# Performance work log

Hardware: AMD Instinct MI355X
Metric: run time of the kernel (lower is better)

## Reference

```python
import jax, jax.numpy as jnp
import numpy as np

# Model dims
B, S, H = 1, 1024, 2048
NH, NKV, DH = 32, 8, 64
G = NH // NKV            # GQA group size
E, K, I = 8, 2, 2048     # experts, top_k, intermediate
ALPHA, LIMIT = 1.702, 7.0
EPS = 1e-5
SCALE = DH ** -0.5


def rmsnorm(x, g):
    return x * jax.lax.rsqrt(jnp.mean(x * x, axis=-1, keepdims=True) + EPS) * g


def setup_inputs() -> dict:
    key = jax.random.key(0)
    ks = jax.random.split(key, 24)
    w = lambda k, shp: jax.random.normal(k, shp, dtype=jnp.float32) * 0.02
    causal = jnp.where(jnp.tril(jnp.ones((S, S), dtype=bool)), 0.0, -1e9).astype(jnp.float32)
    return {
        "hidden_states": jax.random.normal(ks[0], (B, S, H), dtype=jnp.float32),
        "attention_bias": causal[None, None, :, :],           # [1,1,S,S]
        "ln1_g": jnp.ones((H,), jnp.float32),
        "ln2_g": jnp.ones((H,), jnp.float32),
        "Wq": w(ks[1], (NH * DH, H)),  "bq": w(ks[2], (NH * DH,)),
        "Wk": w(ks[3], (NKV * DH, H)), "bk": w(ks[4], (NKV * DH,)),
        "Wv": w(ks[5], (NKV * DH, H)), "bv": w(ks[6], (NKV * DH,)),
        "Wo": w(ks[7], (H, NH * DH)),  "bo": w(ks[8], (H,)),
        "sinks": w(ks[9], (NH,)),
        "router_w": w(ks[10], (E, H)), "router_b": w(ks[11], (E,)),
        "We_gate": w(ks[12], (E, I, H)), "be_gate": w(ks[13], (E, I)),
        "We_up":   w(ks[14], (E, I, H)), "be_up":   w(ks[15], (E, I)),
        "We_down": w(ks[16], (E, H, I)), "be_down": w(ks[17], (E, H)),
    }


def reference(hidden_states, attention_bias, ln1_g, ln2_g,
              Wq, bq, Wk, bk, Wv, bv, Wo, bo, sinks,
              router_w, router_b,
              We_gate, be_gate, We_up, be_up, We_down, be_down):
    x = hidden_states
    # ---- pre-norm sink attention ----
    xn = rmsnorm(x, ln1_g)
    q = (xn @ Wq.T + bq).reshape(B, S, NH, DH).transpose(0, 2, 1, 3)    # [B,NH,S,DH]
    k = (xn @ Wk.T + bk).reshape(B, S, NKV, DH).transpose(0, 2, 1, 3)   # [B,NKV,S,DH]
    v = (xn @ Wv.T + bv).reshape(B, S, NKV, DH).transpose(0, 2, 1, 3)
    # GQA: replicate each kv head G times consecutively (repeat_kv)
    k = jnp.repeat(k, G, axis=1)
    v = jnp.repeat(v, G, axis=1)
    scores = jnp.einsum('bhqd,bhkd->bhqk', q, k) * SCALE + attention_bias  # [B,NH,S,S]
    sink_col = jnp.broadcast_to(sinks.reshape(1, NH, 1, 1), (B, NH, S, 1))
    combined = jnp.concatenate([scores, sink_col], axis=-1)               # [B,NH,S,S+1]
    probs = jax.nn.softmax(combined, axis=-1)[..., :-1]                   # drop sink
    attn = jnp.einsum('bhqk,bhkd->bhqd', probs, v)
    attn = attn.transpose(0, 2, 1, 3).reshape(B, S, NH * DH)
    h = x + (attn @ Wo.T + bo)
    # ---- pre-norm MoE FFN ----
    hn = rmsnorm(h, ln2_g)
    router_logits = hn @ router_w.T + router_b                            # [B,S,E]
    rw, sel = jax.lax.top_k(router_logits, K)
    rw = jax.nn.softmax(rw, axis=-1)                                      # [B,S,K]
    # dense per-expert MLP over all tokens (matches the exported loop)
    gate = jnp.einsum('bsh,eih->bsei', hn, We_gate) + be_gate             # [B,S,E,I]
    up = jnp.einsum('bsh,eih->bsei', hn, We_up) + be_up
    gate_c = jnp.minimum(gate, LIMIT)
    up_c = jnp.clip(up, -LIMIT, LIMIT)
    glu = gate_c * jax.nn.sigmoid(ALPHA * gate_c)
    gated = (up_c + 1.0) * glu
    down = jnp.einsum('bsei,ehi->bseh', gated, We_down) + be_down         # [B,S,E,H]
    # per-token expert weight: sum_k rw * (sel == e)
    wts = jnp.sum(rw[..., None] * (sel[..., None] == jnp.arange(E)), axis=2)  # [B,S,E]
    moe = jnp.einsum('bseh,bse->bsh', down, wts)
    return h + moe
```

## Files before the change

### kernel.cpp

```cpp
#include <hip/hip_runtime.h>
#include <hip/hip_bf16.h>

#define HD 2048
#define SEQ 1024
#define NHEAD 32
#define NKVH 8
#define DHEAD 64
#define NEXP 8
#define INTER 2048
#define SCALE 0.125f
#define ALPHA 1.702f
#define LIMIT 7.0f

typedef __attribute__((ext_vector_type(8))) short short8;
typedef __attribute__((ext_vector_type(4))) short short4v;
typedef __attribute__((ext_vector_type(4))) float f32x4;

__device__ __forceinline__ unsigned short f2bf(float f) {
  union { float f; unsigned u; } v; v.f = f;
  unsigned r = v.u + 0x7fffu + ((v.u >> 16) & 1u);
  return (unsigned short)(r >> 16);
}
__device__ __forceinline__ float bf2f(unsigned short h) {
  union { unsigned u; float f; } v; v.u = ((unsigned)h) << 16; return v.f;
}
__device__ __forceinline__ void split2(float f, unsigned short& hi, unsigned short& lo) {
  hi = f2bf(f);
  lo = f2bf(f - bf2f(hi));
}

__device__ __forceinline__ f32x4 mfma32(short8 a, short8 b, f32x4 c) {
  return __builtin_amdgcn_mfma_f32_16x16x32_bf16(a, b, c, 0, 0, 0);
}

__global__ __launch_bounds__(256) void rmsnorm_split_kernel(
    const float* __restrict__ x, const float* __restrict__ gamma,
    unsigned short* __restrict__ oh, unsigned short* __restrict__ ol) {
  int row = blockIdx.x, tid = threadIdx.x;
  const float* xr = x + (size_t)row * HD;
  float v[8];
#pragma unroll
  for (int i = 0; i < 8; ++i) v[i] = xr[tid * 8 + i];
  float ss = 0.f;
#pragma unroll
  for (int i = 0; i < 8; ++i) ss += v[i] * v[i];
#pragma unroll
  for (int off = 32; off; off >>= 1) ss += __shfl_xor(ss, off, 64);
  __shared__ float wss[4];
  if ((tid & 63) == 0) wss[tid >> 6] = ss;
  __syncthreads();
  float rs = rsqrtf((wss[0] + wss[1] + wss[2] + wss[3]) * (1.0f / HD) + 1e-5f);
  short8 vh, vl;
#pragma unroll
  for (int i = 0; i < 8; ++i) {
    float val = v[i] * rs * gamma[tid * 8 + i];
    unsigned short h, lo;
    split2(val, h, lo);
    vh[i] = (short)h;
    vl[i] = (short)lo;
  }
  *(short8*)(oh + (size_t)row * HD + tid * 8) = vh;
  *(short8*)(ol + (size_t)row * HD + tid * 8) = vl;
}

__global__ __launch_bounds__(256) void rmsnorm_plain_kernel(
    const float* __restrict__ x, const float* __restrict__ gamma,
    unsigned short* __restrict__ out) {
  int row = blockIdx.x, tid = threadIdx.x;
  const float* xr = x + (size_t)row * HD;
  float v[8];
#pragma unroll
  for (int i = 0; i < 8; ++i) v[i] = xr[tid * 8 + i];
  float ss = 0.f;
#pragma unroll
  for (int i = 0; i < 8; ++i) ss += v[i] * v[i];
#pragma unroll
  for (int off = 32; off; off >>= 1) ss += __shfl_xor(ss, off, 64);
  __shared__ float wss[4];
  if ((tid & 63) == 0) wss[tid >> 6] = ss;
  __syncthreads();
  float rs = rsqrtf((wss[0] + wss[1] + wss[2] + wss[3]) * (1.0f / HD) + 1e-5f);
  short8 o;
#pragma unroll
  for (int i = 0; i < 8; ++i) o[i] = (short)f2bf(v[i] * rs * gamma[tid * 8 + i]);
  *(short8*)(out + (size_t)row * HD + tid * 8) = o;
}

template <int MT, int NS, bool SPLIT, int EPI>
__global__ __launch_bounds__(256) void gemm_ws(
    const unsigned short* __restrict__ Ah, const unsigned short* __restrict__ Al,
    int ldA,
    const float* __restrict__ W0, const float* __restrict__ W1,
    const float* __restrict__ W2,
    const float* __restrict__ b0, const float* __restrict__ b1,
    const float* __restrict__ b2,
    const float* __restrict__ resid,
    const int* __restrict__ counts, const int* __restrict__ arows,
    const int* __restrict__ orows,
    unsigned short* __restrict__ oh0, unsigned short* __restrict__ ol0,
    unsigned short* __restrict__ oh1, unsigned short* __restrict__ ol1,
    unsigned short* __restrict__ oh2, unsigned short* __restrict__ ol2,
    float* __restrict__ f0, float* __restrict__ f1,
    int M, int Kd) {
  constexpr int MG = MT * 64;
  constexpr int NR = NS * 16;
  constexpr int TPR = 256 / NR;
  constexpr int CPT = 128 / TPR;
  constexpr int NF4 = CPT / 4;
  constexpr int NPL = SPLIT ? 2 : 1;
  __shared__ __align__(16) unsigned short lw[2][NPL][NR][136];
  int tid = threadIdx.x;
  int l = tid & 63, w = tid >> 6;
  int g = l >> 4, q = l & 15;
  int n0 = blockIdx.x * NR;

  const float* Wb;
  const float* bias;
  int nloc = n0, e = 0, mat = 0;
  if constexpr (EPI == 0) {
    if (n0 < NHEAD * DHEAD) {
      Wb = W0; bias = b0;
    } else if (n0 < NHEAD * DHEAD + NKVH * DHEAD) {
      Wb = W1; bias = b1; nloc = n0 - NHEAD * DHEAD;
    } else {
      Wb = W2; bias = b2; nloc = n0 - (NHEAD * DHEAD + NKVH * DHEAD);
    }
  } else if constexpr (EPI == 1) {
    Wb = W0; bias = b0;
  } else if constexpr (EPI == 2) {
    e = blockIdx.z >> 1;
    mat = blockIdx.z & 1;
    Wb = (mat ? W1 : W0) + (size_t)e * INTER * HD;
    bias = (mat ? b1 : b0) + (size_t)e * INTER;
  } else {
    e = blockIdx.z;
    Wb = W0 + (size_t)e * HD * INTER;
    bias = b0 + (size_t)e * HD;
  }
  int cnt = (EPI >= 2) ? counts[e] : M;
  const float* wrow = Wb + (size_t)(nloc + tid / TPR) * Kd + (tid % TPR) * CPT;
  int wcc = (tid % TPR) * CPT;
  int wrr = tid / TPR;

  float4 wpre[NF4];
  auto stage = [&](int buf) {
#pragma unroll
    for (int j = 0; j < NF4; j += 2) {
      float v[8] = {wpre[j].x,     wpre[j].y,     wpre[j].z,     wpre[j].w,
                    wpre[j + 1].x, wpre[j + 1].y, wpre[j + 1].z, wpre[j + 1].w};
      short8 hh, ll;
#pragma unroll
      for (int jj = 0; jj < 8; ++jj) {
        if constexpr (SPLIT) {
          unsigned short h, lo;
          split2(v[jj], h, lo);
          hh[jj] = (short)h;
          ll[jj] = (short)lo;
        } else {
          hh[jj] = (short)f2bf(v[jj]);
        }
      }
      *(short8*)&lw[buf][0][wrr][wcc + j * 4] = hh;
      if constexpr (SPLIT) *(short8*)&lw[buf][NPL - 1][wrr][wcc + j * 4] = ll;
    }
  };

  for (int mg = blockIdx.y; mg * MG < cnt; mg += gridDim.y) {
    int mb = mg * MG + w * (MT * 16);
    const unsigned short* ap[MT];
    const unsigned short* apl[MT];
#pragma unroll
    for (int mt = 0; mt < MT; ++mt) {
      int mm = min(mb + mt * 16 + q, cnt - 1);
      int ar = (EPI >= 2) ? arows[e * SEQ + mm] : mm;
      ap[mt] = Ah + (size_t)ar * ldA + 8 * g;
      if constexpr (SPLIT) apl[mt] = Al + (size_t)ar * ldA + 8 * g;
    }
    f32x4 acc[MT][NS];
#pragma unroll
    for (int mt = 0; mt < MT; ++mt)
#pragma unroll
      for (int ns = 0; ns < NS; ++ns) acc[mt][ns] = (f32x4){0.f, 0.f, 0.f, 0.f};

#pragma unroll
    for (int j = 0; j < NF4; ++j) wpre[j] = *(const float4*)(wrow + 4 * j);
    short8 ab[2][MT], abl[2][MT];
#pragma unroll
    for (int mt = 0; mt < MT; ++mt) {
      ab[0][mt] = *(const short8*)(ap[mt]);
      ab[1][mt] = *(const short8*)(ap[mt] + 32);
      if constexpr (SPLIT) {
        abl[0][mt] = *(const short8*)(apl[mt]);
        abl[1][mt] = *(const short8*)(apl[mt] + 32);
      }
    }
    stage(0);
    __syncthreads();

    int cb = 0;
    for (int kc = 0; kc < Kd; kc += 128, cb ^= 1) {
      bool more = (kc + 128 < Kd);
      if (more) {
#pragma unroll
        for (int j = 0; j < NF4; ++j)
          wpre[j] = *(const float4*)(wrow + kc + 128 + 4 * j);
      }
#pragma unroll
      for (int kh = 0; kh < 4; ++kh) {
        short8 acur[MT], acl[MT];
#pragma unroll
        for (int mt = 0; mt < MT; ++mt) {
          acur[mt] = ab[kh & 1][mt];
          if constexpr (SPLIT) acl[mt] = abl[kh & 1][mt];
        }
        int kn = kc + kh * 32 + 64;
        if (kn < Kd) {
#pragma unroll
          for (int mt = 0; mt < MT; ++mt) {
            ab[kh & 1][mt] = *(const short8*)(ap[mt] + kn);
            if constexpr (SPLIT) abl[kh & 1][mt] = *(const short8*)(apl[mt] + kn);
          }
        }
        short8 wh[NS], wl[NS];
#pragma unroll
        for (int ns = 0; ns < NS; ++ns) {
          wh[ns] = *(const short8*)&lw[cb][0][ns * 16 + q][kh * 32 + 8 * g];
          if constexpr (SPLIT)
            wl[ns] = *(const short8*)&lw[cb][NPL - 1][ns * 16 + q][kh * 32 + 8 * g];
        }
#pragma unroll
        for (int mt = 0; mt < MT; ++mt)
#pragma unroll
          for (int ns = 0; ns < NS; ++ns) {
            acc[mt][ns] = mfma32(acur[mt], wh[ns], acc[mt][ns]);
            if constexpr (SPLIT) {
              acc[mt][ns] = mfma32(acur[mt], wl[ns], acc[mt][ns]);
              acc[mt][ns] = mfma32(acl[mt], wh[ns], acc[mt][ns]);
            }
          }
      }
      if (more) stage(cb ^ 1);
      __syncthreads();
    }
#pragma unroll
    for (int ns = 0; ns < NS; ++ns) {
      int ncol = nloc + ns * 16 + q;
      float bs = bias[ncol];
#pragma unroll
      for (int mt = 0; mt < MT; ++mt) {
#pragma unroll
        for (int r = 0; r < 4; ++r) {
          int mr = mb + mt * 16 + 4 * g + r;
          float val = acc[mt][ns][r] + bs;
          if constexpr (EPI == 0) {
            unsigned short h, lo;
            split2(val, h, lo);
            if (n0 < NHEAD * DHEAD) {
              oh0[(size_t)mr * (NHEAD * DHEAD) + ncol] = h;
              ol0[(size_t)mr * (NHEAD * DHEAD) + ncol] = lo;
            } else if (n0 < NHEAD * DHEAD + NKVH * DHEAD) {
              oh1[(size_t)mr * (NKVH * DHEAD) + ncol] = h;
              ol1[(size_t)mr * (NKVH * DHEAD) + ncol] = lo;
            } else {
              oh2[(size_t)ncol * SEQ + mr] = h;
              ol2[(size_t)ncol * SEQ + mr] = lo;
            }
          } else if constexpr (EPI == 1) {
            f0[(size_t)mr * HD + ncol] = val + resid[(size_t)mr * HD + ncol];
          } else if constexpr (EPI == 2) {
            if (mr < cnt) {
              int slot = orows[e * SEQ + mr];
              (mat ? f1 : f0)[(size_t)slot * INTER + ncol] = val;
            }
          } else {
            if (mr < cnt) {
              int slot = orows[e * SEQ + mr];
              f0[(size_t)slot * HD + ncol] = val;
            }
          }
        }
      }
    }
  }
}

__global__ __launch_bounds__(256) void attn_kernel(
    const unsigned short* __restrict__ Qh, const unsigned short* __restrict__ Ql,
    const unsigned short* __restrict__ Kh, const unsigned short* __restrict__ Kl,
    const unsigned short* __restrict__ Vh, const unsigned short* __restrict__ Vl,
    const float* __restrict__ sinks, unsigned short* __restrict__ outh,
    unsigned short* __restrict__ outl) {
  __shared__ __align__(16) unsigned short pbuf[4][2][16][40];
  int l = threadIdx.x & 63, widx = threadIdx.x >> 6;
  int wid = blockIdx.x * 4 + widx;
  int head = wid >> 6, qt = wid & 63;
  int q0 = qt * 16;
  int g = l >> 4, q = l & 15;
  int kvh = head >> 2;
  size_t qoff = (size_t)(q0 + q) * (NHEAD * DHEAD) + head * DHEAD + 8 * g;
  short8 qh0 = *(const short8*)(Qh + qoff);
  short8 qh1 = *(const short8*)(Qh + qoff + 32);
  short8 ql0 = *(const short8*)(Ql + qoff);
  short8 ql1 = *(const short8*)(Ql + qoff + 32);
  float m = sinks[head];
  float lsum = 1.0f;
  f32x4 o[4] = {{0, 0, 0, 0}, {0, 0, 0, 0}, {0, 0, 0, 0}, {0, 0, 0, 0}};
  int qglob = q0 + q;
  for (int kt = 0; kt <= qt; kt += 2) {
    bool hasB = (kt + 1) <= qt;
    size_t koff = (size_t)(kt * 16 + q) * (NKVH * DHEAD) + kvh * DHEAD + 8 * g;
    f32x4 stA = {0, 0, 0, 0};
    {
      short8 kh0 = *(const short8*)(Kh + koff);
      short8 kh1 = *(const short8*)(Kh + koff + 32);
      short8 kl0 = *(const short8*)(Kl + koff);
      short8 kl1 = *(const short8*)(Kl + koff + 32);
      stA = mfma32(kh0, qh0, stA);
      stA = mfma32(kh0, ql0, stA);
      stA = mfma32(kl0, qh0, stA);
      stA = mfma32(kh1, qh1, stA);
      stA = mfma32(kh1, ql1, stA);
      stA = mfma32(kl1, qh1, stA);
    }
    f32x4 stB = {0, 0, 0, 0};
    if (hasB) {
      size_t koff2 = koff + (size_t)16 * (NKVH * DHEAD);
      short8 kh0 = *(const short8*)(Kh + koff2);
      short8 kh1 = *(const short8*)(Kh + koff2 + 32);
      short8 kl0 = *(const short8*)(Kl + koff2);
      short8 kl1 = *(const short8*)(Kl + koff2 + 32);
// ... 173 lines not shown
}

extern "C" void kernel_launch(void* const* d_in, const int* in_sizes, int n_in,
                              void* d_out, int out_size, void* d_ws,
                              size_t ws_size, hipStream_t stream) {
  const float* x = (const float*)d_in[0];
  const float* ln1 = (const float*)d_in[2];
  const float* ln2 = (const float*)d_in[3];
  const float* Wq = (const float*)d_in[4];
  const float* bq = (const float*)d_in[5];
  const float* Wk = (const float*)d_in[6];
  const float* bk = (const float*)d_in[7];
  const float* Wv = (const float*)d_in[8];
  const float* bv = (const float*)d_in[9];
  const float* Wo = (const float*)d_in[10];
  const float* bo = (const float*)d_in[11];
  const float* sinks = (const float*)d_in[12];
  const float* rw = (const float*)d_in[13];
  const float* rb = (const float*)d_in[14];
  const float* Wg = (const float*)d_in[15];
  const float* bg = (const float*)d_in[16];
  const float* Wu = (const float*)d_in[17];
  const float* bu = (const float*)d_in[18];
  const float* Wd = (const float*)d_in[19];
  const float* bd = (const float*)d_in[20];
  float* out = (float*)d_out;

  char* ws = (char*)d_ws;
  size_t off = 0;
  auto alloc = [&](size_t bytes) {
    void* p = ws + off;
    off += (bytes + 255) & ~(size_t)255;
    return p;
  };
  unsigned short* xnh = (unsigned short*)alloc((size_t)SEQ * HD * 2);
  unsigned short* xnl = (unsigned short*)alloc((size_t)SEQ * HD * 2);
  unsigned short* qbh = (unsigned short*)alloc((size_t)SEQ * NHEAD * DHEAD * 2);
  unsigned short* qbl = (unsigned short*)alloc((size_t)SEQ * NHEAD * DHEAD * 2);
  unsigned short* kbh = (unsigned short*)alloc((size_t)SEQ * NKVH * DHEAD * 2);
  unsigned short* kbl = (unsigned short*)alloc((size_t)SEQ * NKVH * DHEAD * 2);
  unsigned short* vth = (unsigned short*)alloc((size_t)NKVH * DHEAD * SEQ * 2);
  unsigned short* vtl = (unsigned short*)alloc((size_t)NKVH * DHEAD * SEQ * 2);
  unsigned short* ath = (unsigned short*)alloc((size_t)SEQ * NHEAD * DHEAD * 2);
  unsigned short* atl = (unsigned short*)alloc((size_t)SEQ * NHEAD * DHEAD * 2);
  float* hbuf = (float*)alloc((size_t)SEQ * HD * 4);
  unsigned short* hn = (unsigned short*)alloc((size_t)SEQ * HD * 2);
  float* wsel = (float*)alloc((size_t)SEQ * 2 * 4);
  int* counts = (int*)alloc(NEXP * 4);
  int* lists = (int*)alloc((size_t)NEXP * SEQ * 4);
  int* slotof = (int*)alloc((size_t)NEXP * SEQ * 4);
  float* rawg = (float*)alloc((size_t)2 * SEQ * INTER * 4);
  float* rawu = (float*)alloc((size_t)2 * SEQ * INTER * 4);
  unsigned short* gated = (unsigned short*)alloc((size_t)2 * SEQ * INTER * 2);
  float* scr = rawg;
  (void)ws_size;
  (void)off;

  rmsnorm_split_kernel<<<SEQ, 256, 0, stream>>>(x, ln1, xnh, xnl);
  gemm_ws<4, 2, true, 0><<<dim3(96, 4, 1), 256, 0, stream>>>(
      xnh, xnl, HD, Wq, Wk, Wv, bq, bk, bv, nullptr, nullptr, nullptr, nullptr,
      qbh, qbl, kbh, kbl, vth, vtl, nullptr, nullptr, SEQ, HD);
  attn_kernel<<<NHEAD * 64 / 4, 256, 0, stream>>>(qbh, qbl, kbh, kbl, vth, vtl,
                                                  sinks, ath, atl);
  gemm_ws<4, 2, true, 1><<<dim3(64, 4, 1), 256, 0, stream>>>(
      ath, atl, NHEAD * DHEAD, Wo, nullptr, nullptr, bo, nullptr, nullptr, x,
      nullptr, nullptr, nullptr, nullptr, nullptr, nullptr, nullptr, nullptr,
      nullptr, hbuf, nullptr, SEQ, NHEAD * DHEAD);
  rmsnorm_plain_kernel<<<SEQ, 256, 0, stream>>>(hbuf, ln2, hn);
  hipMemsetAsync(counts, 0, NEXP * sizeof(int), stream);
  router_kernel<<<SEQ, 64, 0, stream>>>(hbuf, ln2, rw, rb, wsel, counts, lists,
                                        slotof);
  gemm_ws<5, 2, false, 2><<<dim3(64, 1, 16), 256, 0, stream>>>(
      hn, nullptr, HD, Wg, Wu, nullptr, bg, bu, nullptr, nullptr, counts, lists,
      slotof, nullptr, nullptr, nullptr, nullptr, nullptr, nullptr, rawg, rawu,
      SEQ, HD);
  act_kernel<<<2 * SEQ, 256, 0, stream>>>(rawg, rawu, gated);
  gemm_ws<5, 2, false, 3><<<dim3(64, 1, 8), 256, 0, stream>>>(
      gated, nullptr, INTER, Wd, nullptr, nullptr, bd, nullptr, nullptr,
      nullptr, counts, slotof, slotof, nullptr, nullptr, nullptr, nullptr,
      nullptr, nullptr, scr, nullptr, SEQ, INTER);
  reduce_kernel<<<SEQ, 256, 0, stream>>>(hbuf, scr, wsel, out);
}
```

Baseline: 663.6 us.

## Pre-convert weights to bf16 and split-K the MoE down projection with atomics

Adds conversion kernels that turn the fp32 weights into bf16 (hi/lo pairs for the attention projections) each call, so the GEMMs load half-width weights without converting inside the kernel. The GEMM inner loop now prefetches two weight chunks into registers with double buffering. The MoE GEMM tiles are widened. The down projection is split across two K halves that accumulate with atomicAdd into a zeroed buffer. The conversion passes add a full extra read and write of all weights on every call, which may cost more than the in-kernel conversion they replace.

```diff
diff --git a/kernel.cpp b/kernel.cpp
--- a/kernel.cpp
+++ b/kernel.cpp
@@ -33,6 +33,35 @@
   return __builtin_amdgcn_mfma_f32_16x16x32_bf16(a, b, c, 0, 0, 0);
 }
 
+__global__ __launch_bounds__(256) void conv_plain(const float* __restrict__ s,
+                                                  unsigned short* __restrict__ d) {
+  size_t i = ((size_t)blockIdx.x * 256 + threadIdx.x) * 8;
+  float4 a = *(const float4*)(s + i), b = *(const float4*)(s + i + 4);
+  float v[8] = {a.x, a.y, a.z, a.w, b.x, b.y, b.z, b.w};
+  short8 o;
+#pragma unroll
+  for (int j = 0; j < 8; ++j) o[j] = (short)f2bf(v[j]);
+  *(short8*)(d + i) = o;
+}
+
+__global__ __launch_bounds__(256) void conv_split(const float* __restrict__ s,
+                                                  unsigned short* __restrict__ dh,
+                                                  unsigned short* __restrict__ dl) {
+  size_t i = ((size_t)blockIdx.x * 256 + threadIdx.x) * 8;
+  float4 a = *(const float4*)(s + i), b = *(const float4*)(s + i + 4);
+  float v[8] = {a.x, a.y, a.z, a.w, b.x, b.y, b.z, b.w};
+  short8 oh, ol;
+#pragma unroll
+  for (int j = 0; j < 8; ++j) {
+    unsigned short h, lo;
+    split2(v[j], h, lo);
+    oh[j] = (short)h;
+    ol[j] = (short)lo;
+  }
+  *(short8*)(dh + i) = oh;
+  *(short8*)(dl + i) = ol;
+}
+
 __global__ __launch_bounds__(256) void rmsnorm_split_kernel(
     const float* __restrict__ x, const float* __restrict__ gamma,
     unsigned short* __restrict__ oh, unsigned short* __restrict__ ol) {
@@ -90,8 +119,9 @@
 __global__ __launch_bounds__(256) void gemm_ws(
     const unsigned short* __restrict__ Ah, const unsigned short* __restrict__ Al,
     int ldA,
-    const float* __restrict__ W0, const float* __restrict__ W1,
-    const float* __restrict__ W2,
+    const unsigned short* __restrict__ W0h, const unsigned short* __restrict__ W0l,
+    const unsigned short* __restrict__ W1h, const unsigned short* __restrict__ W1l,
+    const unsigned short* __restrict__ W2h, const unsigned short* __restrict__ W2l,
     const float* __restrict__ b0, const float* __restrict__ b1,
     const float* __restrict__ b2,
     const float* __restrict__ resid,
@@ -101,12 +131,12 @@
     unsigned short* __restrict__ oh1, unsigned short* __restrict__ ol1,
     unsigned short* __restrict__ oh2, unsigned short* __restrict__ ol2,
     float* __restrict__ f0, float* __restrict__ f1,
-    int M, int Kd) {
+    int M, int Kd, int Kr) {
   constexpr int MG = MT * 64;
   constexpr int NR = NS * 16;
   constexpr int TPR = 256 / NR;
   constexpr int CPT = 128 / TPR;
-  constexpr int NF4 = CPT / 4;
+  constexpr int NW8 = CPT / 8;
   constexpr int NPL = SPLIT ? 2 : 1;
   __shared__ __align__(16) unsigned short lw[2][NPL][NR][136];
   int tid = threadIdx.x;
@@ -114,58 +144,56 @@
   int g = l >> 4, q = l & 15;
   int n0 = blockIdx.x * NR;
 
-  const float* Wb;
+  const unsigned short* Wbh;
+  const unsigned short* Wbl = nullptr;
   const float* bias;
   int nloc = n0, e = 0, mat = 0;
   if constexpr (EPI == 0) {
     if (n0 < NHEAD * DHEAD) {
-      Wb = W0; bias = b0;
+      Wbh = W0h; Wbl = W0l; bias = b0;
     } else if (n0 < NHEAD * DHEAD + NKVH * DHEAD) {
-      Wb = W1; bias = b1; nloc = n0 - NHEAD * DHEAD;
+      Wbh = W1h; Wbl = W1l; bias = b1; nloc = n0 - NHEAD * DHEAD;
     } else {
-      Wb = W2; bias = b2; nloc = n0 - (NHEAD * DHEAD + NKVH * DHEAD);
+      Wbh = W2h; Wbl = W2l; bias = b2; nloc = n0 - (NHEAD * DHEAD + NKVH * DHEAD);
     }
   } else if constexpr (EPI == 1) {
-    Wb = W0; bias = b0;
+    Wbh = W0h; Wbl = W0l; bias = b0;
   } else if constexpr (EPI == 2) {
     e = blockIdx.z >> 1;
     mat = blockIdx.z & 1;
-    Wb = (mat ? W1 : W0) + (size_t)e * INTER * HD;
+    Wbh = (mat ? W1h : W0h) + (size_t)e * INTER * HD;
     bias = (mat ? b1 : b0) + (size_t)e * INTER;
   } else {
     e = blockIdx.z;
-    Wb = W0 + (size_t)e * HD * INTER;
+    Wbh = W0h + (size_t)e * HD * INTER;
     bias = b0 + (size_t)e * HD;
   }
   int cnt = (EPI >= 2) ? counts[e] : M;
-  const float* wrow = Wb + (size_t)(nloc + tid / TPR) * Kd + (tid % TPR) * CPT;
-  int wcc = (tid % TPR) * CPT;
-  int wrr = tid / TPR;
-
-  float4 wpre[NF4];
-  auto stage = [&](int buf) {
-#pragma unroll
-    for (int j = 0; j < NF4; j += 2) {
-      float v[8] = {wpre[j].x,     wpre[j].y,     wpre[j].z,     wpre[j].w,
-                    wpre[j + 1].x, wpre[j + 1].y, wpre[j + 1].z, wpre[j + 1].w};
-      short8 hh, ll;
-#pragma unroll
-      for (int jj = 0; jj < 8; ++jj) {
-        if constexpr (SPLIT) {
-          unsigned short h, lo;
-          split2(v[jj], h, lo);
-          hh[jj] = (short)h;
-          ll[jj] = (short)lo;
-        } else {
-          hh[jj] = (short)f2bf(v[jj]);
-        }
-      }
-      *(short8*)&lw[buf][0][wrr][wcc + j * 4] = hh;
-      if constexpr (SPLIT) *(short8*)&lw[buf][NPL - 1][wrr][wcc + j * 4] = ll;
+  int kstart = (EPI == 3) ? blockIdx.y * Kr : 0;
+  int mstart = (EPI <= 1) ? blockIdx.y : 0;
+  int mstep = (EPI <= 1) ? gridDim.y : 1;
+  int wrr = tid / TPR, wcc = (tid % TPR) * CPT;
+  const unsigned short* wrowh = Wbh + (size_t)(nloc + wrr) * Kd + kstart + wcc;
+  const unsigned short* wrowl =
+      SPLIT ? (Wbl + (size_t)(nloc + wrr) * Kd + kstart + wcc) : nullptr;
+
+  short8 wr[2][NW8], wrl[2][NW8];
+  auto loadW = [&](short8(&dh)[NW8], short8(&dl)[NW8], int kc) {
+#pragma unroll
+    for (int j = 0; j < NW8; ++j) {
+      dh[j] = *(const short8*)(wrowh + kc + j * 8);
+      if constexpr (SPLIT) dl[j] = *(const short8*)(wrowl + kc + j * 8);
     }
   };
-
-  for (int mg = blockIdx.y; mg * MG < cnt; mg += gridDim.y) {
+  auto stage = [&](int buf, short8(&sh)[NW8], short8(&sl)[NW8]) {
+#pragma unroll
+    for (int j = 0; j < NW8; ++j) {
+      *(short8*)&lw[buf][0][wrr][wcc + j * 8] = sh[j];
+      if constexpr (SPLIT) *(short8*)&lw[buf][NPL - 1][wrr][wcc + j * 8] = sl[j];
+    }
+  };
+
+  for (int mg = mstart; mg * MG < cnt; mg += mstep) {
     int mb = mg * MG + w * (MT * 16);
     const unsigned short* ap[MT];
     const unsigned short* apl[MT];
@@ -173,8 +201,8 @@
     for (int mt = 0; mt < MT; ++mt) {
       int mm = min(mb + mt * 16 + q, cnt - 1);
       int ar = (EPI >= 2) ? arows[e * SEQ + mm] : mm;
-      ap[mt] = Ah + (size_t)ar * ldA + 8 * g;
-      if constexpr (SPLIT) apl[mt] = Al + (size_t)ar * ldA + 8 * g;
+      ap[mt] = Ah + (size_t)ar * ldA + kstart + 8 * g;
+      if constexpr (SPLIT) apl[mt] = Al + (size_t)ar * ldA + kstart + 8 * g;
     }
     f32x4 acc[MT][NS];
 #pragma unroll
@@ -182,8 +210,8 @@
 #pragma unroll
       for (int ns = 0; ns < NS; ++ns) acc[mt][ns] = (f32x4){0.f, 0.f, 0.f, 0.f};
 
-#pragma unroll
-    for (int j = 0; j < NF4; ++j) wpre[j] = *(const float4*)(wrow + 4 * j);
+    loadW(wr[0], wrl[0], 0);
+    loadW(wr[1], wrl[1], 128);
     short8 ab[2][MT], abl[2][MT];
 #pragma unroll
     for (int mt = 0; mt < MT; ++mt) {
@@ -194,58 +222,60 @@
         abl[1][mt] = *(const short8*)(apl[mt] + 32);
       }
     }
-    stage(0);
+    stage(0, wr[0], wrl[0]);
     __syncthreads();
 
-    int cb = 0;
-    for (int kc = 0; kc < Kd; kc += 128, cb ^= 1) {
-      bool more = (kc + 128 < Kd);
-      if (more) {
-#pragma unroll
-        for (int j = 0; j < NF4; ++j)
-          wpre[j] = *(const float4*)(wrow + kc + 128 + 4 * j);
-      }
-#pragma unroll
-      for (int kh = 0; kh < 4; ++kh) {
-        short8 acur[MT], acl[MT];
-#pragma unroll
-        for (int mt = 0; mt < MT; ++mt) {
-          acur[mt] = ab[kh & 1][mt];
-          if constexpr (SPLIT) acl[mt] = abl[kh & 1][mt];
-        }
-        int kn = kc + kh * 32 + 64;
-        if (kn < Kd) {
+    for (int kc = 0; kc < Kr; kc += 256) {
+#pragma unroll
+      for (int u = 0; u < 2; ++u) {
+        int kcc = kc + u * 128;
+        if (kcc + 256 < Kr) loadW(wr[u], wrl[u], kcc + 256);
+#pragma unroll
+        for (int kh = 0; kh < 4; ++kh) {
+          short8 acur[MT], acl[MT];
 #pragma unroll
           for (int mt = 0; mt < MT; ++mt) {
-            ab[kh & 1][mt] = *(const short8*)(ap[mt] + kn);
-            if constexpr (SPLIT) abl[kh & 1][mt] = *(const short8*)(apl[mt] + kn);
+            acur[mt] = ab[kh & 1][mt];
+            if constexpr (SPLIT) acl[mt] = abl[kh & 1][mt];
           }
-        }
-        short8 wh[NS], wl[NS];
-#pragma unroll
-        for (int ns = 0; ns < NS; ++ns) {
-          wh[ns] = *(const short8*)&lw[cb][0][ns * 16 + q][kh * 32 + 8 * g];
-          if constexpr (SPLIT)
-            wl[ns] = *(const short8*)&lw[cb][NPL - 1][ns * 16 + q][kh * 32 + 8 * g];
-        }
-#pragma unroll
-        for (int mt = 0; mt < MT; ++mt)
-#pragma unroll
-          for (int ns = 0; ns < NS; ++ns) {
-            acc[mt][ns] = mfma32(acur[mt], wh[ns], acc[mt][ns]);
-            if constexpr (SPLIT) {
-              acc[mt][ns] = mfma32(acur[mt], wl[ns], acc[mt][ns]);
-              acc[mt][ns] = mfma32(acl[mt], wh[ns], acc[mt][ns]);
+          int kn = kcc + kh * 32 + 64;
+          if (kn < Kr) {
+#pragma unroll
+            for (int mt = 0; mt < MT; ++mt) {
+              ab[kh & 1][mt] = *(const short8*)(ap[mt] + kn);
+              if constexpr (SPLIT)
+                abl[kh & 1][mt] = *(const short8*)(apl[mt] + kn);
             }
           }
+          short8 wh[NS], wl[NS];
+#pragma unroll
+          for (int ns = 0; ns < NS; ++ns) {
+            wh[ns] = *(const short8*)&lw[u][0][ns * 16 + q][kh * 32 + 8 * g];
+            if constexpr (SPLIT)
+              wl[ns] = *(const short8*)&lw[u][NPL - 1][ns * 16 + q][kh * 32 + 8 * g];
+          }
+#pragma unroll
+          for (int mt = 0; mt < MT; ++mt)
+#pragma unroll
+            for (int ns = 0; ns < NS; ++ns) {
+              acc[mt][ns] = mfma32(acur[mt], wh[ns], acc[mt][ns]);
+              if constexpr (SPLIT) {
+                acc[mt][ns] = mfma32(acur[mt], wl[ns], acc[mt][ns]);
+                acc[mt][ns] = mfma32(acl[mt], wh[ns], acc[mt][ns]);
+              }
+            }
+        }
+        if (kcc + 128 < Kr) stage(u ^ 1, wr[u ^ 1], wrl[u ^ 1]);
+        __syncthreads();
       }
-      if (more) stage(cb ^ 1);
-      __syncthreads();
     }
 #pragma unroll
     for (int ns = 0; ns < NS; ++ns) {
       int ncol = nloc + ns * 16 + q;
       float bs = bias[ncol];
+      if constexpr (EPI == 3) {
+        if (blockIdx.y != 0) bs = 0.f;
+      }
 #pragma unroll
       for (int mt = 0; mt < MT; ++mt) {
 #pragma unroll
@@ -275,7 +305,7 @@
           } else {
             if (mr < cnt) {
               int slot = orows[e * SEQ + mr];
-              f0[(size_t)slot * HD + ncol] = val;
+              atomicAdd(&f0[(size_t)slot * HD + ncol], val);
             }
           }
         }
@@ -555,32 +585,54 @@
   float* rawg = (float*)alloc((size_t)2 * SEQ * INTER * 4);
   float* rawu = (float*)alloc((size_t)2 * SEQ * INTER * 4);
   unsigned short* gated = (unsigned short*)alloc((size_t)2 * SEQ * INTER * 2);
+  unsigned short* wqh = (unsigned short*)alloc((size_t)HD * HD * 2);
+  unsigned short* wql = (unsigned short*)alloc((size_t)HD * HD * 2);
+  unsigned short* wkh = (unsigned short*)alloc((size_t)NKVH * DHEAD * HD * 2);
+  unsigned short* wkl = (unsigned short*)alloc((size_t)NKVH * DHEAD * HD * 2);
+  unsigned short* wvh = (unsigned short*)alloc((size_t)NKVH * DHEAD * HD * 2);
+  unsigned short* wvl = (unsigned short*)alloc((size_t)NKVH * DHEAD * HD * 2);
+  unsigned short* woh = (unsigned short*)alloc((size_t)HD * HD * 2);
+  unsigned short* wol = (unsigned short*)alloc((size_t)HD * HD * 2);
+  unsigned short* wgb = (unsigned short*)alloc((size_t)NEXP * INTER * HD * 2);
+  unsigned short* wub = (unsigned short*)alloc((size_t)NEXP * INTER * HD * 2);
+  unsigned short* wdb = (unsigned short*)alloc((size_t)NEXP * HD * INTER * 2);
   float* scr = rawg;
   (void)ws_size;
   (void)off;
 
+  conv_split<<<HD * HD / 2048, 256, 0, stream>>>(Wq, wqh, wql);
+  conv_split<<<NKVH * DHEAD * HD / 2048, 256, 0, stream>>>(Wk, wkh, wkl);
+  conv_split<<<NKVH * DHEAD * HD / 2048, 256, 0, stream>>>(Wv, wvh, wvl);
+  conv_split<<<HD * HD / 2048, 256, 0, stream>>>(Wo, woh, wol);
+  conv_plain<<<NEXP * INTER * HD / 2048, 256, 0, stream>>>(Wg, wgb);
+  conv_plain<<<NEXP * INTER * HD / 2048, 256, 0, stream>>>(Wu, wub);
+  conv_plain<<<NEXP * HD * INTER / 2048, 256, 0, stream>>>(Wd, wdb);
+
   rmsnorm_split_kernel<<<SEQ, 256, 0, stream>>>(x, ln1, xnh, xnl);
   gemm_ws<4, 2, true, 0><<<dim3(96, 4, 1), 256, 0, stream>>>(
-      xnh, xnl, HD, Wq, Wk, Wv, bq, bk, bv, nullptr, nullptr, nullptr, nullptr,
-      qbh, qbl, kbh, kbl, vth, vtl, nullptr, nullptr, SEQ, HD);
+      xnh, xnl, HD, wqh, wql, wkh, wkl, wvh, wvl, bq, bk, bv, nullptr, nullptr,
+      nullptr, nullptr, qbh, qbl, kbh, kbl, vth, vtl, nullptr, nullptr, SEQ, HD,
+      HD);
   attn_kernel<<<NHEAD * 64 / 4, 256, 0, stream>>>(qbh, qbl, kbh, kbl, vth, vtl,
                                                   sinks, ath, atl);
   gemm_ws<4, 2, true, 1><<<dim3(64, 4, 1), 256, 0, stream>>>(
-      ath, atl, NHEAD * DHEAD, Wo, nullptr, nullptr, bo, nullptr, nullptr, x,
-      nullptr, nullptr, nullptr, nullptr, nullptr, nullptr, nullptr, nullptr,
-      nullptr, hbuf, nullptr, SEQ, NHEAD * DHEAD);
+      ath, atl, NHEAD * DHEAD, woh, wol, nullptr, nullptr, nullptr, nullptr, bo,
+      nullptr, nullptr, x, nullptr, nullptr, nullptr, nullptr, nullptr, nullptr,
+      nullptr, nullptr, nullptr, hbuf, nullptr, SEQ, NHEAD * DHEAD,
+      NHEAD * DHEAD);
   rmsnorm_plain_kernel<<<SEQ, 256, 0, stream>>>(hbuf, ln2, hn);
   hipMemsetAsync(counts, 0, NEXP * sizeof(int), stream);
   router_kernel<<<SEQ, 64, 0, stream>>>(hbuf, ln2, rw, rb, wsel, counts, lists,
                                         slotof);
-  gemm_ws<5, 2, false, 2><<<dim3(64, 1, 16), 256, 0, stream>>>(
-      hn, nullptr, HD, Wg, Wu, nullptr, bg, bu, nullptr, nullptr, counts, lists,
-      slotof, nullptr, nullptr, nullptr, nullptr, nullptr, nullptr, rawg, rawu,
-      SEQ, HD);
+  gemm_ws<4, 4, false, 2><<<dim3(32, 1, 16), 256, 0, stream>>>(
+      hn, nullptr, HD, wgb, nullptr, wub, nullptr, nullptr, nullptr, bg, bu,
+      nullptr, nullptr, counts, lists, slotof, nullptr, nullptr, nullptr,
+      nullptr, nullptr, nullptr, rawg, rawu, SEQ, HD, HD);
   act_kernel<<<2 * SEQ, 256, 0, stream>>>(rawg, rawu, gated);
-  gemm_ws<5, 2, false, 3><<<dim3(64, 1, 8), 256, 0, stream>>>(
-      gated, nullptr, INTER, Wd, nullptr, nullptr, bd, nullptr, nullptr,
-      nullptr, counts, slotof, slotof, nullptr, nullptr, nullptr, nullptr,
-      nullptr, nullptr, scr, nullptr, SEQ, INTER);
+  hipMemsetAsync(scr, 0, (size_t)2 * SEQ * HD * 4, stream);
+  gemm_ws<4, 4, false, 3><<<dim3(32, 2, 8), 256, 0, stream>>>(
+      gated, nullptr, INTER, wdb, nullptr, nullptr, nullptr, nullptr, nullptr,
+      bd, nullptr, nullptr, nullptr, counts, slotof, slotof, nullptr, nullptr,
+      nullptr, nullptr, nullptr, nullptr, scr, nullptr, SEQ, INTER, INTER / 2);
   reduce_kernel<<<SEQ, 256, 0, stream>>>(hbuf, scr, wsel, out);
 }
```

Result: slower. 779.4 us (+17.5%).

## Stage MoE expert weights via direct global-to-LDS loads with swizzled fp32 tiles

Applied to the files above, without the earlier changes.

Adds a new grouped GEMM kernel for the MoE gate/up and down projections. It uses global_load_lds to copy fp32 weight tiles straight into XOR-swizzled shared memory, double-buffered over 64-wide K chunks, and converts them to bf16 when each MFMA fragment is read. This removes the register round trip and per-thread conversion at staging time. The gate/up launch also moves to 64-row N tiles. The dense gemm_ws loses its routed paths and its weight-load mapping is reworked for coalescing. The cost is repeated bf16 conversion per LDS read, double the LDS footprint for fp32 tiles, and a full sync per 64-K chunk.

```diff
diff --git a/kernel.cpp b/kernel.cpp
--- a/kernel.cpp
+++ b/kernel.cpp
@@ -33,6 +33,12 @@
   return __builtin_amdgcn_mfma_f32_16x16x32_bf16(a, b, c, 0, 0, 0);
 }
 
+__device__ __forceinline__ void gl_lds16(const float* g, float* l) {
+  __builtin_amdgcn_global_load_lds(
+      (const __attribute__((address_space(1))) unsigned int*)g,
+      (__attribute__((address_space(3))) unsigned int*)l, 16, 0, 0);
+}
+
 __global__ __launch_bounds__(256) void rmsnorm_split_kernel(
     const float* __restrict__ x, const float* __restrict__ gamma,
     unsigned short* __restrict__ oh, unsigned short* __restrict__ ol) {
@@ -95,8 +101,6 @@
     const float* __restrict__ b0, const float* __restrict__ b1,
     const float* __restrict__ b2,
     const float* __restrict__ resid,
-    const int* __restrict__ counts, const int* __restrict__ arows,
-    const int* __restrict__ orows,
     unsigned short* __restrict__ oh0, unsigned short* __restrict__ ol0,
     unsigned short* __restrict__ oh1, unsigned short* __restrict__ ol1,
     unsigned short* __restrict__ oh2, unsigned short* __restrict__ ol2,
@@ -104,9 +108,7 @@
     int M, int Kd) {
   constexpr int MG = MT * 64;
   constexpr int NR = NS * 16;
-  constexpr int TPR = 256 / NR;
-  constexpr int CPT = 128 / TPR;
-  constexpr int NF4 = CPT / 4;
+  constexpr int NF4 = NR / 8;
   constexpr int NPL = SPLIT ? 2 : 1;
   __shared__ __align__(16) unsigned short lw[2][NPL][NR][136];
   int tid = threadIdx.x;
@@ -116,7 +118,7 @@
 
   const float* Wb;
   const float* bias;
-  int nloc = n0, e = 0, mat = 0;
+  int nloc = n0;
   if constexpr (EPI == 0) {
     if (n0 < NHEAD * DHEAD) {
       Wb = W0; bias = b0;
@@ -125,32 +127,27 @@
     } else {
       Wb = W2; bias = b2; nloc = n0 - (NHEAD * DHEAD + NKVH * DHEAD);
     }
-  } else if constexpr (EPI == 1) {
+  } else {
     Wb = W0; bias = b0;
-  } else if constexpr (EPI == 2) {
-    e = blockIdx.z >> 1;
-    mat = blockIdx.z & 1;
-    Wb = (mat ? W1 : W0) + (size_t)e * INTER * HD;
-    bias = (mat ? b1 : b0) + (size_t)e * INTER;
-  } else {
-    e = blockIdx.z;
-    Wb = W0 + (size_t)e * HD * INTER;
-    bias = b0 + (size_t)e * HD;
-  }
-  int cnt = (EPI >= 2) ? counts[e] : M;
-  const float* wrow = Wb + (size_t)(nloc + tid / TPR) * Kd + (tid % TPR) * CPT;
-  int wcc = (tid % TPR) * CPT;
-  int wrr = tid / TPR;
+  }
+  int wrow_j[NF4];
+  int wcolf = (l & 31) * 4;
+  const float* wptr[NF4];
+#pragma unroll
+  for (int j = 0; j < NF4; ++j) {
+    int r = 2 * (w * NF4 + j) + (l >> 5);
+    wrow_j[j] = r;
+    wptr[j] = Wb + (size_t)(nloc + r) * Kd + wcolf;
+  }
 
   float4 wpre[NF4];
   auto stage = [&](int buf) {
 #pragma unroll
-    for (int j = 0; j < NF4; j += 2) {
-      float v[8] = {wpre[j].x,     wpre[j].y,     wpre[j].z,     wpre[j].w,
-                    wpre[j + 1].x, wpre[j + 1].y, wpre[j + 1].z, wpre[j + 1].w};
-      short8 hh, ll;
-#pragma unroll
-      for (int jj = 0; jj < 8; ++jj) {
+    for (int j = 0; j < NF4; ++j) {
+      float v[4] = {wpre[j].x, wpre[j].y, wpre[j].z, wpre[j].w};
+      short4v hh, ll;
+#pragma unroll
+      for (int jj = 0; jj < 4; ++jj) {
         if constexpr (SPLIT) {
           unsigned short h, lo;
           split2(v[jj], h, lo);
@@ -160,21 +157,20 @@
           hh[jj] = (short)f2bf(v[jj]);
         }
       }
-      *(short8*)&lw[buf][0][wrr][wcc + j * 4] = hh;
-      if constexpr (SPLIT) *(short8*)&lw[buf][NPL - 1][wrr][wcc + j * 4] = ll;
+      *(short4v*)&lw[buf][0][wrow_j[j]][wcolf] = hh;
+      if constexpr (SPLIT) *(short4v*)&lw[buf][NPL - 1][wrow_j[j]][wcolf] = ll;
     }
   };
 
-  for (int mg = blockIdx.y; mg * MG < cnt; mg += gridDim.y) {
+  for (int mg = blockIdx.y; mg * MG < M; mg += gridDim.y) {
     int mb = mg * MG + w * (MT * 16);
     const unsigned short* ap[MT];
     const unsigned short* apl[MT];
 #pragma unroll
     for (int mt = 0; mt < MT; ++mt) {
-      int mm = min(mb + mt * 16 + q, cnt - 1);
-      int ar = (EPI >= 2) ? arows[e * SEQ + mm] : mm;
-      ap[mt] = Ah + (size_t)ar * ldA + 8 * g;
-      if constexpr (SPLIT) apl[mt] = Al + (size_t)ar * ldA + 8 * g;
+      int mm = mb + mt * 16 + q;
+      ap[mt] = Ah + (size_t)mm * ldA + 8 * g;
+      if constexpr (SPLIT) apl[mt] = Al + (size_t)mm * ldA + 8 * g;
     }
     f32x4 acc[MT][NS];
 #pragma unroll
@@ -183,7 +179,7 @@
       for (int ns = 0; ns < NS; ++ns) acc[mt][ns] = (f32x4){0.f, 0.f, 0.f, 0.f};
 
 #pragma unroll
-    for (int j = 0; j < NF4; ++j) wpre[j] = *(const float4*)(wrow + 4 * j);
+    for (int j = 0; j < NF4; ++j) wpre[j] = *(const float4*)(wptr[j]);
     short8 ab[2][MT], abl[2][MT];
 #pragma unroll
     for (int mt = 0; mt < MT; ++mt) {
@@ -203,7 +199,7 @@
       if (more) {
 #pragma unroll
         for (int j = 0; j < NF4; ++j)
-          wpre[j] = *(const float4*)(wrow + kc + 128 + 4 * j);
+          wpre[j] = *(const float4*)(wptr[j] + kc + 128);
       }
 #pragma unroll
       for (int kh = 0; kh < 4; ++kh) {
@@ -265,16 +261,140 @@
               oh2[(size_t)ncol * SEQ + mr] = h;
               ol2[(size_t)ncol * SEQ + mr] = lo;
             }
-          } else if constexpr (EPI == 1) {
+          } else {
             f0[(size_t)mr * HD + ncol] = val + resid[(size_t)mr * HD + ncol];
-          } else if constexpr (EPI == 2) {
-            if (mr < cnt) {
-              int slot = orows[e * SEQ + mr];
+          }
+        }
+      }
+    }
+  }
+}
+
+template <int MT, int NS, int EPI>
+__global__ __launch_bounds__(256) void gemm_gl(
+    const unsigned short* __restrict__ A, int ldA,
+    const float* __restrict__ W0, const float* __restrict__ W1,
+    const float* __restrict__ b0f, const float* __restrict__ b1f,
+    const int* __restrict__ counts, const int* __restrict__ arows,
+    const int* __restrict__ orows,
+    float* __restrict__ f0, float* __restrict__ f1, int Kd) {
+  constexpr int NR = NS * 16;
+  constexpr int RPW = NR / 4;
+  constexpr int NI = RPW / 4;
+  __shared__ __align__(16) float lw[2][NR][64];
+  int tid = threadIdx.x, l = tid & 63, w = tid >> 6;
+  int g = l >> 4, q = l & 15;
+  int e, mat = 0;
+  if constexpr (EPI == 2) {
+    e = blockIdx.z >> 1;
+    mat = blockIdx.z & 1;
+  } else {
+    e = blockIdx.z;
+  }
+  int n0 = blockIdx.x * NR;
+  const float* Wb;
+  const float* bias;
+  if constexpr (EPI == 2) {
+    Wb = (mat ? W1 : W0) + (size_t)e * INTER * HD;
+    bias = (mat ? b1f : b0f) + (size_t)e * INTER;
+  } else {
+    Wb = W0 + (size_t)e * HD * INTER;
+    bias = b0f + (size_t)e * HD;
+  }
+  int cnt = counts[e];
+
+  const float* sptr[NI];
+  float* sdst0[NI];
+  float* sdst1[NI];
+#pragma unroll
+  for (int j = 0; j < NI; ++j) {
+    int r = RPW * w + 4 * j + (l >> 4);
+    int gs = ((l & 15) ^ ((4 * j + (l >> 4)) & 7)) * 4;
+    sptr[j] = Wb + (size_t)(n0 + r) * Kd + gs;
+    sdst0[j] = &lw[0][RPW * w + 4 * j][0];
+    sdst1[j] = &lw[1][RPW * w + 4 * j][0];
+  }
+  auto stage = [&](int buf, int kc) {
+#pragma unroll
+    for (int j = 0; j < NI; ++j)
+      gl_lds16(sptr[j] + kc, buf ? sdst1[j] : sdst0[j]);
+  };
+
+  for (int mg = 0; mg * (MT * 64) < cnt; ++mg) {
+    int mb = mg * (MT * 64) + w * (MT * 16);
+    const unsigned short* ap[MT];
+#pragma unroll
+    for (int mt = 0; mt < MT; ++mt) {
+      int mm = min(mb + mt * 16 + q, cnt - 1);
+      ap[mt] = A + (size_t)arows[e * SEQ + mm] * ldA + 8 * g;
+    }
+    f32x4 acc[MT][NS];
+#pragma unroll
+    for (int mt = 0; mt < MT; ++mt)
+#pragma unroll
+      for (int ns = 0; ns < NS; ++ns) acc[mt][ns] = (f32x4){0.f, 0.f, 0.f, 0.f};
+
+    stage(0, 0);
+    short8 ab[2][MT];
+#pragma unroll
+    for (int mt = 0; mt < MT; ++mt) {
+      ab[0][mt] = *(const short8*)(ap[mt]);
+      ab[1][mt] = *(const short8*)(ap[mt] + 32);
+    }
+    __syncthreads();
+
+    int nc = Kd / 64;
+    for (int c = 0; c < nc; ++c) {
+      int u = c & 1;
+      if (c + 1 < nc) stage(u ^ 1, (c + 1) * 64);
+#pragma unroll
+      for (int kh = 0; kh < 2; ++kh) {
+        short8 acur[MT];
+#pragma unroll
+        for (int mt = 0; mt < MT; ++mt) acur[mt] = ab[kh][mt];
+        int kn = c * 64 + kh * 32 + 64;
+        if (kn < Kd) {
+#pragma unroll
+          for (int mt = 0; mt < MT; ++mt)
+            ab[kh][mt] = *(const short8*)(ap[mt] + kn);
+        }
+        short8 wf[NS];
+#pragma unroll
+        for (int ns = 0; ns < NS; ++ns) {
+          int row = ns * 16 + q;
+          int r7 = q & 7;
+          int i0 = ((kh * 8 + g * 2) ^ r7) * 16;
+          int i1 = ((kh * 8 + g * 2 + 1) ^ r7) * 16;
+          const char* base = (const char*)&lw[u][row][0];
+          float4 v0 = *(const float4*)(base + i0);
+          float4 v1 = *(const float4*)(base + i1);
+          float vv[8] = {v0.x, v0.y, v0.z, v0.w, v1.x, v1.y, v1.z, v1.w};
+#pragma unroll
+          for (int jj = 0; jj < 8; ++jj) wf[ns][jj] = (short)f2bf(vv[jj]);
+        }
+#pragma unroll
+        for (int mt = 0; mt < MT; ++mt)
+#pragma unroll
+          for (int ns = 0; ns < NS; ++ns)
+            acc[mt][ns] = mfma32(acur[mt], wf[ns], acc[mt][ns]);
+      }
+      __syncthreads();
+    }
+#pragma unroll
+    for (int ns = 0; ns < NS; ++ns) {
+      int ncol = n0 + ns * 16 + q;
+      float bs = bias[ncol];
+#pragma unroll
+      for (int mt = 0; mt < MT; ++mt) {
+#pragma unroll
+        for (int r = 0; r < 4; ++r) {
+          int mr = mb + mt * 16 + 4 * g + r;
+          if (mr < cnt) {
+            int slot = orows[e * SEQ + mr];
+            float val = acc[mt][ns][r] + bs;
+            if constexpr (EPI == 2) {
               (mat ? f1 : f0)[(size_t)slot * INTER + ncol] = val;
-            }
-          } else {
-            if (mr < cnt) {
-              int slot = orows[e * SEQ + mr];
+            } else {
               f0[(size_t)slot * HD + ncol] = val;
             }
           }
@@ -561,26 +681,23 @@
 
   rmsnorm_split_kernel<<<SEQ, 256, 0, stream>>>(x, ln1, xnh, xnl);
   gemm_ws<4, 2, true, 0><<<dim3(96, 4, 1), 256, 0, stream>>>(
-      xnh, xnl, HD, Wq, Wk, Wv, bq, bk, bv, nullptr, nullptr, nullptr, nullptr,
-      qbh, qbl, kbh, kbl, vth, vtl, nullptr, nullptr, SEQ, HD);
+      xnh, xnl, HD, Wq, Wk, Wv, bq, bk, bv, nullptr, qbh, qbl, kbh, kbl, vth,
+      vtl, nullptr, nullptr, SEQ, HD);
   attn_kernel<<<NHEAD * 64 / 4, 256, 0, stream>>>(qbh, qbl, kbh, kbl, vth, vtl,
                                                   sinks, ath, atl);
   gemm_ws<4, 2, true, 1><<<dim3(64, 4, 1), 256, 0, stream>>>(
       ath, atl, NHEAD * DHEAD, Wo, nullptr, nullptr, bo, nullptr, nullptr, x,
-      nullptr, nullptr, nullptr, nullptr, nullptr, nullptr, nullptr, nullptr,
-      nullptr, hbuf, nullptr, SEQ, NHEAD * DHEAD);
+      nullptr, nullptr, nullptr, nullptr, nullptr, nullptr, hbuf, nullptr, SEQ,
+      NHEAD * DHEAD);
   rmsnorm_plain_kernel<<<SEQ, 256, 0, stream>>>(hbuf, ln2, hn);
   hipMemsetAsync(counts, 0, NEXP * sizeof(int), stream);
   router_kernel<<<SEQ, 64, 0, stream>>>(hbuf, ln2, rw, rb, wsel, counts, lists,
                                         slotof);
-  gemm_ws<5, 2, false, 2><<<dim3(64, 1, 16), 256, 0, stream>>>(
-      hn, nullptr, HD, Wg, Wu, nullptr, bg, bu, nullptr, nullptr, counts, lists,
-      slotof, nullptr, nullptr, nullptr, nullptr, nullptr, nullptr, rawg, rawu,
-      SEQ, HD);
+  gemm_gl<5, 4, 2><<<dim3(32, 1, 16), 256, 0, stream>>>(
+      hn, HD, Wg, Wu, bg, bu, counts, lists, slotof, rawg, rawu, HD);
   act_kernel<<<2 * SEQ, 256, 0, stream>>>(rawg, rawu, gated);
-  gemm_ws<5, 2, false, 3><<<dim3(64, 1, 8), 256, 0, stream>>>(
-      gated, nullptr, INTER, Wd, nullptr, nullptr, bd, nullptr, nullptr,
-      nullptr, counts, slotof, slotof, nullptr, nullptr, nullptr, nullptr,
-      nullptr, nullptr, scr, nullptr, SEQ, INTER);
+  gemm_gl<5, 2, 3><<<dim3(64, 1, 8), 256, 0, stream>>>(
+      gated, INTER, Wd, nullptr, bd, nullptr, counts, slotof, slotof, scr,
+      nullptr, INTER);
   reduce_kernel<<<SEQ, 256, 0, stream>>>(hbuf, scr, wsel, out);
 }
```

Measured after the change: 610.8 us. 1.09x faster.

## Stage fp32 weights via direct global-to-LDS loads and convert at fragment read

Applied to the files above, without the earlier changes.

Replaces the register-staged weight path (global float4 load, bf16 split, LDS store) with async global_load_lds copies of raw fp32 weight tiles into an XOR-swizzled LDS buffer. Conversion to bf16 hi/lo now happens when each wave reads its MFMA fragment, and the K chunk shrinks from 128 to 64. The expert gate/up GEMM also moves to NS=4 with half the column blocks. This is meant to cut VGPR pressure and load-to-LDS latency in the weight-bandwidth-bound GEMMs. The cost is repeated conversion work per wave, because each wave converts the same weights redundantly.

```diff
diff --git a/kernel.cpp b/kernel.cpp
--- a/kernel.cpp
+++ b/kernel.cpp
@@ -33,6 +33,12 @@
   return __builtin_amdgcn_mfma_f32_16x16x32_bf16(a, b, c, 0, 0, 0);
 }
 
+__device__ __forceinline__ void gl_lds16(const float* g, float* l) {
+  __builtin_amdgcn_global_load_lds(
+      (const __attribute__((address_space(1))) unsigned int*)g,
+      (__attribute__((address_space(3))) unsigned int*)l, 16, 0, 0);
+}
+
 __global__ __launch_bounds__(256) void rmsnorm_split_kernel(
     const float* __restrict__ x, const float* __restrict__ gamma,
     unsigned short* __restrict__ oh, unsigned short* __restrict__ ol) {
@@ -87,7 +93,7 @@
 }
 
 template <int MT, int NS, bool SPLIT, int EPI>
-__global__ __launch_bounds__(256) void gemm_ws(
+__global__ __launch_bounds__(256) void gemm_gl(
     const unsigned short* __restrict__ Ah, const unsigned short* __restrict__ Al,
     int ldA,
     const float* __restrict__ W0, const float* __restrict__ W1,
@@ -104,13 +110,10 @@
     int M, int Kd) {
   constexpr int MG = MT * 64;
   constexpr int NR = NS * 16;
-  constexpr int TPR = 256 / NR;
-  constexpr int CPT = 128 / TPR;
-  constexpr int NF4 = CPT / 4;
-  constexpr int NPL = SPLIT ? 2 : 1;
-  __shared__ __align__(16) unsigned short lw[2][NPL][NR][136];
-  int tid = threadIdx.x;
-  int l = tid & 63, w = tid >> 6;
+  constexpr int RPW = NR / 4;
+  constexpr int NI = RPW / 4;
+  __shared__ __align__(16) float lw[2][NR][64];
+  int tid = threadIdx.x, l = tid & 63, w = tid >> 6;
   int g = l >> 4, q = l & 15;
   int n0 = blockIdx.x * NR;
 
@@ -138,34 +141,28 @@
     bias = b0 + (size_t)e * HD;
   }
   int cnt = (EPI >= 2) ? counts[e] : M;
-  const float* wrow = Wb + (size_t)(nloc + tid / TPR) * Kd + (tid % TPR) * CPT;
-  int wcc = (tid % TPR) * CPT;
-  int wrr = tid / TPR;
-
-  float4 wpre[NF4];
-  auto stage = [&](int buf) {
-#pragma unroll
-    for (int j = 0; j < NF4; j += 2) {
-      float v[8] = {wpre[j].x,     wpre[j].y,     wpre[j].z,     wpre[j].w,
-                    wpre[j + 1].x, wpre[j + 1].y, wpre[j + 1].z, wpre[j + 1].w};
-      short8 hh, ll;
-#pragma unroll
-      for (int jj = 0; jj < 8; ++jj) {
-        if constexpr (SPLIT) {
-          unsigned short h, lo;
-          split2(v[jj], h, lo);
-          hh[jj] = (short)h;
-          ll[jj] = (short)lo;
-        } else {
-          hh[jj] = (short)f2bf(v[jj]);
-        }
-      }
-      *(short8*)&lw[buf][0][wrr][wcc + j * 4] = hh;
-      if constexpr (SPLIT) *(short8*)&lw[buf][NPL - 1][wrr][wcc + j * 4] = ll;
-    }
+
+  const float* sptr[NI];
+  float* sdst0[NI];
+  float* sdst1[NI];
+#pragma unroll
+  for (int j = 0; j < NI; ++j) {
+    int r = RPW * w + 4 * j + (l >> 4);
+    int gs = ((l & 15) ^ (r & 7)) * 4;
+    sptr[j] = Wb + (size_t)(nloc + r) * Kd + gs;
+    sdst0[j] = &lw[0][RPW * w + 4 * j][0];
+    sdst1[j] = &lw[1][RPW * w + 4 * j][0];
+  }
+  auto stage = [&](int buf, int kc) {
+#pragma unroll
+    for (int j = 0; j < NI; ++j)
+      gl_lds16(sptr[j] + kc, buf ? sdst1[j] : sdst0[j]);
   };
 
-  for (int mg = blockIdx.y; mg * MG < cnt; mg += gridDim.y) {
+  int mstart = (EPI <= 1) ? blockIdx.y : 0;
+  int mstep = (EPI <= 1) ? gridDim.y : 1;
+
+  for (int mg = mstart; mg * MG < cnt; mg += mstep) {
     int mb = mg * MG + w * (MT * 16);
     const unsigned short* ap[MT];
     const unsigned short* apl[MT];
@@ -182,8 +179,7 @@
 #pragma unroll
       for (int ns = 0; ns < NS; ++ns) acc[mt][ns] = (f32x4){0.f, 0.f, 0.f, 0.f};
 
-#pragma unroll
-    for (int j = 0; j < NF4; ++j) wpre[j] = *(const float4*)(wrow + 4 * j);
+    stage(0, 0);
     short8 ab[2][MT], abl[2][MT];
 #pragma unroll
     for (int mt = 0; mt < MT; ++mt) {
@@ -194,39 +190,50 @@
         abl[1][mt] = *(const short8*)(apl[mt] + 32);
       }
     }
-    stage(0);
     __syncthreads();
 
-    int cb = 0;
-    for (int kc = 0; kc < Kd; kc += 128, cb ^= 1) {
-      bool more = (kc + 128 < Kd);
-      if (more) {
-#pragma unroll
-        for (int j = 0; j < NF4; ++j)
-          wpre[j] = *(const float4*)(wrow + kc + 128 + 4 * j);
-      }
-#pragma unroll
-      for (int kh = 0; kh < 4; ++kh) {
+    int nc = Kd / 64;
+    for (int c = 0; c < nc; ++c) {
+      int u = c & 1;
+      if (c + 1 < nc) stage(u ^ 1, (c + 1) * 64);
+#pragma unroll
+      for (int kh = 0; kh < 2; ++kh) {
         short8 acur[MT], acl[MT];
 #pragma unroll
         for (int mt = 0; mt < MT; ++mt) {
-          acur[mt] = ab[kh & 1][mt];
-          if constexpr (SPLIT) acl[mt] = abl[kh & 1][mt];
+          acur[mt] = ab[kh][mt];
+          if constexpr (SPLIT) acl[mt] = abl[kh][mt];
         }
-        int kn = kc + kh * 32 + 64;
+        int kn = c * 64 + kh * 32 + 64;
         if (kn < Kd) {
 #pragma unroll
           for (int mt = 0; mt < MT; ++mt) {
-            ab[kh & 1][mt] = *(const short8*)(ap[mt] + kn);
-            if constexpr (SPLIT) abl[kh & 1][mt] = *(const short8*)(apl[mt] + kn);
+            ab[kh][mt] = *(const short8*)(ap[mt] + kn);
+            if constexpr (SPLIT) abl[kh][mt] = *(const short8*)(apl[mt] + kn);
           }
         }
         short8 wh[NS], wl[NS];
 #pragma unroll
         for (int ns = 0; ns < NS; ++ns) {
-          wh[ns] = *(const short8*)&lw[cb][0][ns * 16 + q][kh * 32 + 8 * g];
-          if constexpr (SPLIT)
-            wl[ns] = *(const short8*)&lw[cb][NPL - 1][ns * 16 + q][kh * 32 + 8 * g];
+          int row = ns * 16 + q;
+          int r7 = q & 7;
+          int i0 = ((kh * 8 + g * 2) ^ r7) * 16;
+          int i1 = ((kh * 8 + g * 2 + 1) ^ r7) * 16;
+          const char* base = (const char*)&lw[u][row][0];
+          float4 v0 = *(const float4*)(base + i0);
+          float4 v1 = *(const float4*)(base + i1);
+          float vv[8] = {v0.x, v0.y, v0.z, v0.w, v1.x, v1.y, v1.z, v1.w};
+#pragma unroll
+          for (int jj = 0; jj < 8; ++jj) {
+            if constexpr (SPLIT) {
+              unsigned short h, lo;
+              split2(vv[jj], h, lo);
+              wh[ns][jj] = (short)h;
+              wl[ns][jj] = (short)lo;
+            } else {
+              wh[ns][jj] = (short)f2bf(vv[jj]);
+            }
+          }
         }
 #pragma unroll
         for (int mt = 0; mt < MT; ++mt)
@@ -239,7 +246,6 @@
             }
           }
       }
-      if (more) stage(cb ^ 1);
       __syncthreads();
     }
 #pragma unroll
@@ -560,12 +566,12 @@
   (void)off;
 
   rmsnorm_split_kernel<<<SEQ, 256, 0, stream>>>(x, ln1, xnh, xnl);
-  gemm_ws<4, 2, true, 0><<<dim3(96, 4, 1), 256, 0, stream>>>(
+  gemm_gl<4, 2, true, 0><<<dim3(96, 4, 1), 256, 0, stream>>>(
       xnh, xnl, HD, Wq, Wk, Wv, bq, bk, bv, nullptr, nullptr, nullptr, nullptr,
       qbh, qbl, kbh, kbl, vth, vtl, nullptr, nullptr, SEQ, HD);
   attn_kernel<<<NHEAD * 64 / 4, 256, 0, stream>>>(qbh, qbl, kbh, kbl, vth, vtl,
                                                   sinks, ath, atl);
-  gemm_ws<4, 2, true, 1><<<dim3(64, 4, 1), 256, 0, stream>>>(
+  gemm_gl<4, 2, true, 1><<<dim3(64, 4, 1), 256, 0, stream>>>(
       ath, atl, NHEAD * DHEAD, Wo, nullptr, nullptr, bo, nullptr, nullptr, x,
       nullptr, nullptr, nullptr, nullptr, nullptr, nullptr, nullptr, nullptr,
       nullptr, hbuf, nullptr, SEQ, NHEAD * DHEAD);
@@ -573,12 +579,12 @@
   hipMemsetAsync(counts, 0, NEXP * sizeof(int), stream);
   router_kernel<<<SEQ, 64, 0, stream>>>(hbuf, ln2, rw, rb, wsel, counts, lists,
                                         slotof);
-  gemm_ws<5, 2, false, 2><<<dim3(64, 1, 16), 256, 0, stream>>>(
+  gemm_gl<5, 4, false, 2><<<dim3(32, 1, 16), 256, 0, stream>>>(
       hn, nullptr, HD, Wg, Wu, nullptr, bg, bu, nullptr, nullptr, counts, lists,
       slotof, nullptr, nullptr, nullptr, nullptr, nullptr, nullptr, rawg, rawu,
       SEQ, HD);
   act_kernel<<<2 * SEQ, 256, 0, stream>>>(rawg, rawu, gated);
-  gemm_ws<5, 2, false, 3><<<dim3(64, 1, 8), 256, 0, stream>>>(
+  gemm_gl<5, 2, false, 3><<<dim3(64, 1, 8), 256, 0, stream>>>(
       gated, nullptr, INTER, Wd, nullptr, nullptr, bd, nullptr, nullptr,
       nullptr, counts, slotof, slotof, nullptr, nullptr, nullptr, nullptr,
       nullptr, nullptr, scr, nullptr, SEQ, INTER);
```

Result: faster. 606.6 us (-8.6%).
